# Optimization experiments

Hardware: AMD Instinct MI355X
Metric: run time of the kernel (lower is better)

The kernel has to match this reference:

```python
import jax, jax.numpy as jnp
import numpy as np


def setup_inputs() -> dict:
    key = jax.random.key(0)
    k1, k2 = jax.random.split(key)
    N, D, O, K = 65536, 256, 256, 8  # tokens, inputdim, outdim, degree+1
    gridsize = 8
    x = jax.random.normal(k1, (N, D), dtype=jnp.float32)
    # init stddev = 1/(sqrt(inputdim)*sqrt(gridsize)) as in the module
    std = 1.0 / (np.sqrt(D) * np.sqrt(gridsize))
    cheby_coeffs = jax.random.normal(k2, (O, D, K), dtype=jnp.float32) * std
    bias = jnp.zeros((1, O), dtype=jnp.float32)
    return {"x": x, "cheby_coeffs": cheby_coeffs, "bias": bias}


def reference(x, cheby_coeffs, bias):
    # x: (N, D); cheby_coeffs: (O, D, K); bias: (1, O)
    K = cheby_coeffs.shape[-1]
    xt = jnp.tanh(x)                       # squash into [-1, 1]
    theta = jnp.arccos(xt)                 # (N, D)
    n = jnp.arange(K, dtype=x.dtype)       # Chebyshev orders 0..degree
    # T_n(xt) = cos(n * arccos(xt)), matching the original per-degree loop
    T = jnp.cos(theta[..., None] * n)      # (N, D, K)
    y = jnp.einsum('ndk,odk->no', T, cheby_coeffs)  # (N, O)
    y = y + bias
    return y
```

## Files before the change

### kernel.cpp

```cpp
#include <hip/hip_runtime.h>
#include <hip/hip_bf16.h>

typedef __attribute__((ext_vector_type(4)))  int   i32x4;
typedef __attribute__((ext_vector_type(16))) int   i32x16;

#define DIM_D 256
#define DIM_O 256
#define DIM_K 8
#define BM 128
#define NCHUNK 16
#define NSTEP 4
#define MAGIC 12582912.f

__global__ __launch_bounds__(256) void pack_w_kernel(
    const float* __restrict__ coeffs,
    unsigned int* __restrict__ wp,
    float* __restrict__ scales)
{
    const int o = blockIdx.x;
    const int d = threadIdx.x;
    const float* cp = coeffs + ((size_t)o * DIM_D + d) * DIM_K;
    float4 c0 = *(const float4*)cp;
    float4 c1 = *(const float4*)(cp + 4);

    float m = fmaxf(fmaxf(fmaxf(fabsf(c0.x), fabsf(c0.y)),
                          fmaxf(fabsf(c0.z), fabsf(c0.w))),
                    fmaxf(fmaxf(fabsf(c1.x), fabsf(c1.y)),
                          fmaxf(fabsf(c1.z), fabsf(c1.w))));
    #pragma unroll
    for (int i = 32; i >= 1; i >>= 1)
        m = fmaxf(m, __shfl_xor(m, i));
    __shared__ float wm[4];
    if ((d & 63) == 0) wm[d >> 6] = m;
    __syncthreads();
    const float sc = fmaxf(fmaxf(fmaxf(wm[0], wm[1]), fmaxf(wm[2], wm[3])),
                           1e-30f);
    if (d == 0) scales[o] = sc;

    const float inv = 127.0f / sc;
    unsigned f0 = __float_as_uint(__builtin_fmaf(c0.x, inv, MAGIC));
    unsigned f1 = __float_as_uint(__builtin_fmaf(c0.y, inv, MAGIC));
    unsigned f2 = __float_as_uint(__builtin_fmaf(c0.z, inv, MAGIC));
    unsigned f3 = __float_as_uint(__builtin_fmaf(c0.w, inv, MAGIC));
    unsigned f4 = __float_as_uint(__builtin_fmaf(c1.x, inv, MAGIC));
    unsigned f5 = __float_as_uint(__builtin_fmaf(c1.y, inv, MAGIC));
    unsigned f6 = __float_as_uint(__builtin_fmaf(c1.z, inv, MAGIC));
    unsigned f7 = __float_as_uint(__builtin_fmaf(c1.w, inv, MAGIC));
    unsigned rA = __builtin_amdgcn_perm(f1, f0, 0x00000400u);
    unsigned rB = __builtin_amdgcn_perm(f3, f2, 0x00000400u);
    unsigned rC = __builtin_amdgcn_perm(f5, f4, 0x00000400u);
    unsigned rD = __builtin_amdgcn_perm(f7, f6, 0x00000400u);
    unsigned lo = __builtin_amdgcn_perm(rB, rA, 0x05040100u);
    unsigned hi = __builtin_amdgcn_perm(rD, rC, 0x05040100u);

    const int base = (((d >> 2) * 8 + (o >> 5)) * 64
                      + ((d >> 1) & 1) * 32 + (o & 31)) * 4 + (d & 1) * 2;
    wp[base]     = lo;
    wp[base + 1] = hi;
}

__device__ __forceinline__ void cheb_q8(float xs, unsigned int* o2) {
    float e2 = __expf(2.f * xs);
    float r  = __builtin_amdgcn_rcpf(e2 + 1.f);
    float T1 = __builtin_fmaf(-2.f, r, 1.f);
    float tx = T1 + T1;
    float T2 = __builtin_fmaf(tx, T1, -1.f);
    float T3 = __builtin_fmaf(tx, T2, -T1);
    float T4 = __builtin_fmaf(tx, T3, -T2);
    float T5 = __builtin_fmaf(tx, T4, -T3);
    float T6 = __builtin_fmaf(tx, T5, -T4);
    float T7 = __builtin_fmaf(tx, T6, -T5);
    unsigned f1 = __float_as_uint(__builtin_fmaf(T1, 127.f, MAGIC));
    unsigned f2 = __float_as_uint(__builtin_fmaf(T2, 127.f, MAGIC));
    unsigned f3 = __float_as_uint(__builtin_fmaf(T3, 127.f, MAGIC));
    unsigned f4 = __float_as_uint(__builtin_fmaf(T4, 127.f, MAGIC));
    unsigned f5 = __float_as_uint(__builtin_fmaf(T5, 127.f, MAGIC));
    unsigned f6 = __float_as_uint(__builtin_fmaf(T6, 127.f, MAGIC));
    unsigned f7 = __float_as_uint(__builtin_fmaf(T7, 127.f, MAGIC));
    unsigned rA = __builtin_amdgcn_perm(f2, f1, 0x00000400u);
    unsigned rC = __builtin_amdgcn_perm(f5, f4, 0x00000400u);
    unsigned rD = __builtin_amdgcn_perm(f7, f6, 0x00000400u);
    o2[0] = __builtin_amdgcn_perm(f3, rA, 0x0401000Cu) | 127u;
    o2[1] = __builtin_amdgcn_perm(rD, rC, 0x05040100u);
}

__global__ __launch_bounds__(512, 4) void cfkan_kernel(
    const float* __restrict__ x,
    const i32x4* __restrict__ wp8,
    const float* __restrict__ scales,
    const float* __restrict__ bias,
    float* __restrict__ y)
{
    __shared__ unsigned char Abuf[2][BM][128];

    const int t = threadIdx.x;
    const int wid = t >> 6;
    const int wc = wid & 3;
    const int wr = wid >> 2;
    const int l = t & 63;
    const int m = l & 31;
    const int h = l >> 5;
    const int row0 = blockIdx.x * BM;

    i32x16 acc[2][2];
    #pragma unroll
    for (int rt = 0; rt < 2; ++rt)
        #pragma unroll
        for (int ct = 0; ct < 2; ++ct)
            #pragma unroll
            for (int qi = 0; qi < 16; ++qi)
                acc[rt][ct][qi] = 0;

    const int lrow = t >> 2;
    const int tq   = t & 3;
    const float* xrow = x + (size_t)(row0 + lrow) * DIM_D + tq * 4;

#define READA(DST, AB, S) do {                                             \
    const int _so = (((2 * (S) + h) ^ (m & 7)) * 16);                      \
    DST[0] = *(const i32x4*)&AB[wr * 64 +      m][_so];                    \
    DST[1] = *(const i32x4*)&AB[wr * 64 + 32 + m][_so];                    \
} while (0)
#define LOADB2(DST, SG) do {                                               \
    DST[0] = wp8[((SG) * 8 + wc * 2 + 0) * 64 + l];                        \
    DST[1] = wp8[((SG) * 8 + wc * 2 + 1) * 64 + l];                        \
} while (0)
#define STAGE2(ANX, J, X0, X1) do {                                        \
    union { unsigned int u[4]; i32x4 v; } _tv;                             \
    cheb_q8(X0, &_tv.u[0]);                                                \
    cheb_q8(X1, &_tv.u[2]);                                                \
    *(i32x4*)&ANX[lrow][(((tq * 2 + (J)) ^ (lrow & 7)) * 16)] = _tv.v;     \
} while (0)
#define SOFT_BARRIER() do {                                                \
    asm volatile("s_waitcnt lgkmcnt(0)" ::: "memory");                     \
    __builtin_amdgcn_s_barrier();                                          \
    __builtin_amdgcn_sched_barrier(0);                                     \
} while (0)

    {
        float4 xc = *(const float4*)xrow;
        STAGE2(Abuf[0], 0, xc.x, xc.y);
        STAGE2(Abuf[0], 1, xc.z, xc.w);
    }
    float4 xv = *(const float4*)(xrow + 16);
    i32x4 bc[2], bn[2];
    LOADB2(bc, 0);
    SOFT_BARRIER();
    i32x4 r[2], rn[2];
    READA(r, Abuf[0], 0);

    #pragma unroll 1
    for (int c = 0; c < NCHUNK; ++c) {
        const unsigned char (*A)[128] = Abuf[c & 1];
        unsigned char (*ANX)[128]     = Abuf[(c & 1) ^ 1];
        const bool stage = (c < NCHUNK - 1);
        float4 xn;
        if (c + 2 < NCHUNK)
            xn = *(const float4*)(xrow + (c + 2) * 16);

        #pragma unroll
        for (int s = 0; s < NSTEP; ++s) {
            LOADB2(bn, (c * 4 + s + 1) & 63);
            if (s < NSTEP - 1) READA(rn, A, s + 1);

            __builtin_amdgcn_s_setprio(1);
            acc[0][0] = __builtin_amdgcn_mfma_i32_32x32x32_i8(
                r[0], bc[0], acc[0][0], 0, 0, 0);
            acc[0][1] = __builtin_amdgcn_mfma_i32_32x32x32_i8(
                r[0], bc[1], acc[0][1], 0, 0, 0);
            acc[1][0] = __builtin_amdgcn_mfma_i32_32x32x32_i8(
                r[1], bc[0], acc[1][0], 0, 0, 0);
            acc[1][1] = __builtin_amdgcn_mfma_i32_32x32x32_i8(
                r[1], bc[1], acc[1][1], 0, 0, 0);
            __builtin_amdgcn_s_setprio(0);

            if (s == 1 && stage) STAGE2(ANX, 0, xv.x, xv.y);
            if (s == 3 && stage) STAGE2(ANX, 1, xv.z, xv.w);

            if (s < NSTEP - 1) { r[0] = rn[0]; r[1] = rn[1]; }
            bc[0] = bn[0]; bc[1] = bn[1];
        }
        if (c + 2 < NCHUNK) xv = xn;

        SOFT_BARRIER();
        if (c < NCHUNK - 1) READA(r, ANX, 0);
    }

    #pragma unroll
    for (int ct = 0; ct < 2; ++ct) {
        const int col = wc * 64 + ct * 32 + m;
        const float sf = scales[col] * (1.f / 16129.f);
        const float bv = bias[col];
        #pragma unroll
        for (int rt = 0; rt < 2; ++rt) {
            #pragma unroll
            for (int qi = 0; qi < 16; ++qi) {
                const int grow = row0 + wr * 64 + rt * 32
                               + (qi & 3) + 8 * (qi >> 2) + 4 * h;
                y[(size_t)grow * DIM_O + col] =
                    __builtin_fmaf((float)acc[rt][ct][qi], sf, bv);
            }
        }
    }
#undef READA
#undef LOADB2
#undef STAGE2
#undef SOFT_BARRIER
}

extern "C" void kernel_launch(void* const* d_in, const int* in_sizes, int n_in,
                              void* d_out, int out_size, void* d_ws, size_t ws_size,
                              hipStream_t stream) {
    const float* x      = (const float*)d_in[0];
    const float* coeffs = (const float*)d_in[1];
    const float* bias   = (const float*)d_in[2];
    float* y = (float*)d_out;
    float*        scales = (float*)d_ws;
    unsigned int* wp     = (unsigned int*)((char*)d_ws + 1024);

    const int n_tokens = in_sizes[0] / DIM_D;

    pack_w_kernel<<<DIM_O, 256, 0, stream>>>(coeffs, wp, scales);
    cfkan_kernel<<<n_tokens / BM, 512, 0, stream>>>(
        x, (const i32x4*)wp, scales, bias, y);
}
```

Baseline: 56.97 us.

## Compute Chebyshev A fragments in registers per wave, dropping LDS staging

```diff
diff --git a/kernel.cpp b/kernel.cpp
--- a/kernel.cpp
+++ b/kernel.cpp
@@ -8,8 +8,6 @@
 #define DIM_O 256
 #define DIM_K 8
 #define BM 128
-#define NCHUNK 16
-#define NSTEP 4
 #define MAGIC 12582912.f
 
 __global__ __launch_bounds__(256) void pack_w_kernel(
@@ -84,127 +82,107 @@
     o2[1] = __builtin_amdgcn_perm(rD, rC, 0x05040100u);
 }
 
-__global__ __launch_bounds__(512, 4) void cfkan_kernel(
+__device__ __forceinline__ i32x4 chebA(float2 xp) {
+    union { unsigned int u[4]; i32x4 v; } tv;
+    cheb_q8(xp.x, &tv.u[0]);
+    cheb_q8(xp.y, &tv.u[2]);
+    return tv.v;
+}
+
+__global__ __launch_bounds__(256, 2) void cfkan_kernel(
     const float* __restrict__ x,
     const i32x4* __restrict__ wp8,
     const float* __restrict__ scales,
     const float* __restrict__ bias,
     float* __restrict__ y)
 {
-    __shared__ unsigned char Abuf[2][BM][128];
-
     const int t = threadIdx.x;
-    const int wid = t >> 6;
-    const int wc = wid & 3;
-    const int wr = wid >> 2;
+    const int w = t >> 6;
     const int l = t & 63;
     const int m = l & 31;
     const int h = l >> 5;
-    const int row0 = blockIdx.x * BM;
-
-    i32x16 acc[2][2];
+    const int bid = (int)blockIdx.x;
+    const int cpx = (int)gridDim.x >> 3;
+    const int tok0 = ((bid & 7) * cpx + (bid >> 3)) * BM + w * 32;
+    const float* xl = x + (size_t)(tok0 + m) * DIM_D + h * 2;
+    const i32x4* wl = wp8 + l;
+
+    i32x16 acc[8];
     #pragma unroll
-    for (int rt = 0; rt < 2; ++rt)
+    for (int ct = 0; ct < 8; ++ct)
         #pragma unroll
-        for (int ct = 0; ct < 2; ++ct)
-            #pragma unroll
-            for (int qi = 0; qi < 16; ++qi)
-                acc[rt][ct][qi] = 0;
-
-    const int lrow = t >> 2;
-    const int tq   = t & 3;
-    const float* xrow = x + (size_t)(row0 + lrow) * DIM_D + tq * 4;
-
-#define READA(DST, AB, S) do {                                             \
-    const int _so = (((2 * (S) + h) ^ (m & 7)) * 16);                      \
-    DST[0] = *(const i32x4*)&AB[wr * 64 +      m][_so];                    \
-    DST[1] = *(const i32x4*)&AB[wr * 64 + 32 + m][_so];                    \
+        for (int qi = 0; qi < 16; ++qi)
+            acc[ct][qi] = 0;
+
+#define LOADW(DST, SG) do {                                                \
+    DST[0] = wl[((SG) * 8 + 0) * 64];                                      \
+    DST[1] = wl[((SG) * 8 + 1) * 64];                                      \
+    DST[2] = wl[((SG) * 8 + 2) * 64];                                      \
+    DST[3] = wl[((SG) * 8 + 3) * 64];                                      \
+    DST[4] = wl[((SG) * 8 + 4) * 64];                                      \
+    DST[5] = wl[((SG) * 8 + 5) * 64];                                      \
+    DST[6] = wl[((SG) * 8 + 6) * 64];                                      \
+    DST[7] = wl[((SG) * 8 + 7) * 64];                                      \
 } while (0)
-#define LOADB2(DST, SG) do {                                               \
-    DST[0] = wp8[((SG) * 8 + wc * 2 + 0) * 64 + l];                        \
-    DST[1] = wp8[((SG) * 8 + wc * 2 + 1) * 64 + l];                        \
+#define MFMA8(WB, AA) do {                                                 \
+    __builtin_amdgcn_s_setprio(1);                                         \
+    _Pragma("unroll")                                                      \
+    for (int _ct = 0; _ct < 8; ++_ct)                                      \
+        acc[_ct] = __builtin_amdgcn_mfma_i32_32x32x32_i8(                  \
+            AA, WB[_ct], acc[_ct], 0, 0, 0);                               \
+    __builtin_amdgcn_s_setprio(0);                                         \
 } while (0)
-#define STAGE2(ANX, J, X0, X1) do {                                        \
-    union { unsigned int u[4]; i32x4 v; } _tv;                             \
-    cheb_q8(X0, &_tv.u[0]);                                                \
-    cheb_q8(X1, &_tv.u[2]);                                                \
-    *(i32x4*)&ANX[lrow][(((tq * 2 + (J)) ^ (lrow & 7)) * 16)] = _tv.v;     \
+#define LOADX(V0, V1, V2, V3, C) do {                                      \
+    V0 = *(const float2*)(xl + 16 * (C));                                  \
+    V1 = *(const float2*)(xl + 16 * (C) + 4);                              \
+    V2 = *(const float2*)(xl + 16 * (C) + 8);                              \
+    V3 = *(const float2*)(xl + 16 * (C) + 12);                             \
 } while (0)
-#define SOFT_BARRIER() do {                                                \
-    asm volatile("s_waitcnt lgkmcnt(0)" ::: "memory");                     \
-    __builtin_amdgcn_s_barrier();                                          \
-    __builtin_amdgcn_sched_barrier(0);                                     \
-} while (0)
-
-    {
-        float4 xc = *(const float4*)xrow;
-        STAGE2(Abuf[0], 0, xc.x, xc.y);
-        STAGE2(Abuf[0], 1, xc.z, xc.w);
+
+    float2 xc0, xc1, xc2, xc3, xn0, xn1, xn2, xn3;
+    LOADX(xc0, xc1, xc2, xc3, 0);
+    i32x4 W0[8], W1[8];
+    LOADW(W0, 0);
+    i32x4 A0 = chebA(xc0);
+    i32x4 A1;
+
+    #pragma unroll 1
+    for (int c = 0; c < 16; ++c) {
+        const int s0 = c * 4;
+        const int cn = (c + 1 < 16) ? c + 1 : 15;
+        LOADX(xn0, xn1, xn2, xn3, cn);
+
+        LOADW(W1, s0 + 1);
+        A1 = chebA(xc1);
+        MFMA8(W0, A0);
+        LOADW(W0, s0 + 2);
+        A0 = chebA(xc2);
+        MFMA8(W1, A1);
+        LOADW(W1, s0 + 3);
+        A1 = chebA(xc3);
+        MFMA8(W0, A0);
+        LOADW(W0, (s0 + 4) & 63);
+        A0 = chebA(xn0);
+        MFMA8(W1, A1);
+
+        xc0 = xn0; xc1 = xn1; xc2 = xn2; xc3 = xn3;
     }
-    float4 xv = *(const float4*)(xrow + 16);
-    i32x4 bc[2], bn[2];
-    LOADB2(bc, 0);
-    SOFT_BARRIER();
-    i32x4 r[2], rn[2];
-    READA(r, Abuf[0], 0);
-
-    #pragma unroll 1
-    for (int c = 0; c < NCHUNK; ++c) {
-        const unsigned char (*A)[128] = Abuf[c & 1];
-        unsigned char (*ANX)[128]     = Abuf[(c & 1) ^ 1];
-        const bool stage = (c < NCHUNK - 1);
-        float4 xn;
-        if (c + 2 < NCHUNK)
-            xn = *(const float4*)(xrow + (c + 2) * 16);
-
-        #pragma unroll
-        for (int s = 0; s < NSTEP; ++s) {
-            LOADB2(bn, (c * 4 + s + 1) & 63);
-            if (s < NSTEP - 1) READA(rn, A, s + 1);
-
-            __builtin_amdgcn_s_setprio(1);
-            acc[0][0] = __builtin_amdgcn_mfma_i32_32x32x32_i8(
-                r[0], bc[0], acc[0][0], 0, 0, 0);
-            acc[0][1] = __builtin_amdgcn_mfma_i32_32x32x32_i8(
-                r[0], bc[1], acc[0][1], 0, 0, 0);
-            acc[1][0] = __builtin_amdgcn_mfma_i32_32x32x32_i8(
-                r[1], bc[0], acc[1][0], 0, 0, 0);
-            acc[1][1] = __builtin_amdgcn_mfma_i32_32x32x32_i8(
-                r[1], bc[1], acc[1][1], 0, 0, 0);
-            __builtin_amdgcn_s_setprio(0);
-
-            if (s == 1 && stage) STAGE2(ANX, 0, xv.x, xv.y);
-            if (s == 3 && stage) STAGE2(ANX, 1, xv.z, xv.w);
-
-            if (s < NSTEP - 1) { r[0] = rn[0]; r[1] = rn[1]; }
-            bc[0] = bn[0]; bc[1] = bn[1];
-        }
-        if (c + 2 < NCHUNK) xv = xn;
-
-        SOFT_BARRIER();
-        if (c < NCHUNK - 1) READA(r, ANX, 0);
-    }
 
     #pragma unroll
-    for (int ct = 0; ct < 2; ++ct) {
-        const int col = wc * 64 + ct * 32 + m;
+    for (int ct = 0; ct < 8; ++ct) {
+        const int col = ct * 32 + m;
         const float sf = scales[col] * (1.f / 16129.f);
         const float bv = bias[col];
         #pragma unroll
-        for (int rt = 0; rt < 2; ++rt) {
-            #pragma unroll
-            for (int qi = 0; qi < 16; ++qi) {
-                const int grow = row0 + wr * 64 + rt * 32
-                               + (qi & 3) + 8 * (qi >> 2) + 4 * h;
-                y[(size_t)grow * DIM_O + col] =
-                    __builtin_fmaf((float)acc[rt][ct][qi], sf, bv);
-            }
+        for (int qi = 0; qi < 16; ++qi) {
+            const int grow = tok0 + (qi & 3) + 8 * (qi >> 2) + 4 * h;
+            y[(size_t)grow * DIM_O + col] =
+                __builtin_fmaf((float)acc[ct][qi], sf, bv);
         }
     }
-#undef READA
-#undef LOADB2
-#undef STAGE2
-#undef SOFT_BARRIER
+#undef LOADW
+#undef MFMA8
+#undef LOADX
 }
 
 extern "C" void kernel_launch(void* const* d_in, const int* in_sizes, int n_in,
@@ -220,6 +198,6 @@
     const int n_tokens = in_sizes[0] / DIM_D;
 
     pack_w_kernel<<<DIM_O, 256, 0, stream>>>(coeffs, wp, scales);
-    cfkan_kernel<<<n_tokens / BM, 512, 0, stream>>>(
+    cfkan_kernel<<<n_tokens / BM, 256, 0, stream>>>(
         x, (const i32x4*)wp, scales, bias, y);
 }
```

Measured after the change: 67.06 us. 1.18x slower.
